# Kernel optimization log

Hardware: AMD Instinct MI355X
Metric: run time of the kernel (lower is better)

The kernel has to match this reference:

```python
import jax, jax.numpy as jnp
import numpy as np

NUM_HEADS = 16
EMBED_DIM = 1024
WINDOW = 8  # attention_window: corner blocks masked with -inf


def _corner_mask(seq_len, w, dtype):
    # zeros everywhere, -inf in top-left [w,w] and bottom-right [w,w] blocks
    m = jnp.zeros((seq_len, seq_len), dtype=dtype)
    neg_inf = jnp.asarray(-jnp.inf, dtype)
    m = m.at[:w, :w].set(neg_inf)
    m = m.at[-w:, -w:].set(neg_inf)
    return m  # [S, S]


def setup_inputs() -> dict:
    key = jax.random.key(0)
    ks = jax.random.split(key, 7)
    B, S, D = 2, 2048, EMBED_DIM
    sc = 0.02
    return {
        "x": jax.random.normal(ks[0], (B, S, D), jnp.float32),
        "Wq": jax.random.normal(ks[1], (D, D), jnp.float32) * sc,
        "bq": jnp.zeros((D,), jnp.float32),
        "Wk": jax.random.normal(ks[2], (D, D), jnp.float32) * sc,
        "bk": jnp.zeros((D,), jnp.float32),
        "Wv": jax.random.normal(ks[3], (D, D), jnp.float32) * sc,
        "bv": jnp.zeros((D,), jnp.float32),
        "global_bias": jnp.zeros((1, NUM_HEADS, 1, 1), jnp.float32),
    }


def reference(x, Wq, bq, Wk, bk, Wv, bv, global_bias):
    B, S, D = x.shape
    H = NUM_HEADS
    hd = D // H
    # linear projections (torch nn.Linear: x @ W.T + b)
    q = (x @ Wq.T + bq).reshape(B, S, H, hd).transpose(0, 2, 1, 3)  # [B,H,S,hd]
    k = (x @ Wk.T + bk).reshape(B, S, H, hd).transpose(0, 2, 1, 3)
    v = (x @ Wv.T + bv).reshape(B, S, H, hd).transpose(0, 2, 1, 3)
    # NOTE: source scales by sqrt(embed_dim), not sqrt(head_dim)
    scores = jnp.einsum("bhqd,bhkd->bhqk", q, k) / jnp.sqrt(jnp.asarray(D, x.dtype))
    scores = scores + global_bias  # learned per-head scalar bias
    scores = scores + _corner_mask(S, WINDOW, x.dtype)  # broadcast [S,S] -> [B,H,S,S]
    attn = jax.nn.softmax(scores, axis=-1)
    ctx = jnp.einsum("bhqk,bhkd->bhqd", attn, v)  # [B,H,S,hd]
    return ctx.transpose(0, 2, 1, 3).reshape(B, S, D)
```

## Files before the change

kernel.cpp:

```cpp
#include <hip/hip_runtime.h>

#define SEQ 2048
#define HDIM 64
#define NH 16
#define EMB 1024

typedef __attribute__((ext_vector_type(8))) short bf16x8;
typedef __attribute__((ext_vector_type(4))) float f32x4;
typedef __attribute__((ext_vector_type(16))) float f32x16;

static __device__ __forceinline__ unsigned short f2bf(float f) {
  unsigned int u = __builtin_bit_cast(unsigned int, f);
  u += 0x7FFF + ((u >> 16) & 1);
  return (unsigned short)(u >> 16);
}

__global__ void cvt_bf16(const float* __restrict__ in, unsigned short* __restrict__ out, int n) {
  int i = (blockIdx.x * blockDim.x + threadIdx.x) * 4;
  if (i + 3 < n) {
    float4 v = *(const float4*)(in + i);
    ushort4 o;
    o.x = f2bf(v.x); o.y = f2bf(v.y); o.z = f2bf(v.z); o.w = f2bf(v.w);
    *(ushort4*)(out + i) = o;
  }
}

__global__ __launch_bounds__(256) void qkv_gemm(
    const unsigned short* __restrict__ xb,
    const unsigned short* __restrict__ wb,
    const float* __restrict__ bq, const float* __restrict__ bk, const float* __restrict__ bv,
    unsigned short* __restrict__ qout, unsigned short* __restrict__ kout,
    unsigned short* __restrict__ vtout)
{
  __shared__ unsigned short As[3][128 * 32];
  __shared__ unsigned short Bs[3][128 * 32];
  const int bid = blockIdx.x;
  const int xg = bid & 7, jj0 = bid >> 3;
  const int cl = jj0 / 24, kk = jj0 % 24;
  const int chunk = xg * 4 + cl;
  const int mg = chunk >> 3, sg = chunk & 7;
  const int mt = mg * 8 + (kk & 7);
  const int strip = sg * 3 + (kk >> 3);
  const int z = strip >> 3;
  const int m0 = mt * 128, n0 = (strip & 7) * 128;

  const unsigned short* Bw = wb + (size_t)z * (EMB * EMB);
  const int tid = threadIdx.x;
  const int w = tid >> 6, l = tid & 63;
  const int wr = w >> 1, wc = w & 1;
  const int lc = l & 15, lg = l >> 4;
  const int NK = EMB / 32;

  f32x4 acc[4][4] = {};

  auto stage = [&](int buf, int kb) {
#pragma unroll
    for (int c = 0; c < 2; ++c) {
      int elem = c * 2048 + w * 512 + l * 8;
      int row = elem >> 5, col = elem & 31;
      __builtin_amdgcn_global_load_lds(
          (const __attribute__((address_space(1))) void*)(xb + (size_t)(m0 + row) * EMB + kb + col),
          (__attribute__((address_space(3))) void*)(&As[buf][c * 2048 + w * 512]), 16, 0, 0);
      __builtin_amdgcn_global_load_lds(
          (const __attribute__((address_space(1))) void*)(Bw + (size_t)(n0 + row) * EMB + kb + col),
          (__attribute__((address_space(3))) void*)(&Bs[buf][c * 2048 + w * 512]), 16, 0, 0);
    }
  };

  stage(0, 0);
  stage(1, 32);

  int cur = 0;
  for (int t = 0; t < NK; ++t) {
    if (t + 1 < NK) {
      asm volatile("s_waitcnt vmcnt(4)" ::: "memory");
    } else {
      asm volatile("s_waitcnt vmcnt(0)" ::: "memory");
    }
    __builtin_amdgcn_s_barrier();
    __builtin_amdgcn_sched_barrier(0);
    bf16x8 am[4], bn[4];
#pragma unroll
    for (int i = 0; i < 4; ++i) {
      am[i] = *(const bf16x8*)(&As[cur][(wr * 64 + i * 16 + lc) * 32 + lg * 8]);
      bn[i] = *(const bf16x8*)(&Bs[cur][(wc * 64 + i * 16 + lc) * 32 + lg * 8]);
    }
    if (t + 2 < NK) {
      int nb = cur + 2; if (nb >= 3) nb -= 3;
      stage(nb, (t + 2) * 32);
    }
#pragma unroll
    for (int i = 0; i < 4; ++i)
#pragma unroll
      for (int j = 0; j < 4; ++j)
        acc[i][j] = __builtin_amdgcn_mfma_f32_16x16x32_bf16(am[i], bn[j], acc[i][j], 0, 0, 0);
    ++cur; if (cur >= 3) cur = 0;
  }

  const float* bias = (z == 0) ? bq : (z == 1) ? bk : bv;
  const float qscale = 0.03125f * 1.44269504f;
  for (int i = 0; i < 4; ++i)
    for (int j = 0; j < 4; ++j)
      for (int r = 0; r < 4; ++r) {
        int m = m0 + wr * 64 + i * 16 + lg * 4 + r;
        int n = n0 + wc * 64 + j * 16 + lc;
        float v = acc[i][j][r] + bias[n];
        if (z == 0) v *= qscale;
        unsigned short o16 = f2bf(v);
        int b = m >> 11, s = m & 2047, h = n >> 6, d = n & 63;
        if (z == 2) {
          int sz = (s & ~12) | ((s & 4) << 1) | ((s & 8) >> 1);
          vtout[(((size_t)b * NH + h) * HDIM + d) * SEQ + sz] = o16;
        } else {
          unsigned short* dst = (z == 0) ? qout : kout;
          dst[(((size_t)b * NH + h) * SEQ + s) * HDIM + d] = o16;
        }
      }
}

__global__ __launch_bounds__(512, 4) void attn(
    const unsigned short* __restrict__ Q,
    const unsigned short* __restrict__ K,
    const unsigned short* __restrict__ VT,
    float* __restrict__ out)
{
  __shared__ __align__(16) unsigned char ldsraw[34816];
  const int g = blockIdx.x;
  const int xcd = g & 7, j0 = g >> 3;
  const int bh = xcd * 4 + (j0 >> 4);
  const int qt = j0 & 15;
  const int b = bh >> 4, h = bh & 15;
  const int tid = threadIdx.x;
  const int half = tid >> 8;
  const int wv4 = (tid >> 6) & 3;
  const int l = tid & 63;
  const int q = l & 31;
  const int hh = l >> 5;
  const int q0 = qt * 128 + wv4 * 32;
  const int NBLK = (SEQ / 2) / 32;

  unsigned short* kv0 = (unsigned short*)ldsraw + half * 8192;
  unsigned short* kv1 = kv0 + 4096;

  const unsigned short* Qp = Q + ((size_t)bh * SEQ + q0) * HDIM;
  const unsigned short* Kp = K + ((size_t)bh * SEQ + (size_t)half * (SEQ / 2)) * HDIM;
  const unsigned short* Vp = VT + (size_t)bh * HDIM * SEQ + (size_t)half * (SEQ / 2);

  bf16x8 qf[4];
#pragma unroll
  for (int c = 0; c < 4; ++c)
    qf[c] = *(const bf16x8*)(Qp + q * HDIM + c * 16 + hh * 8);

  uint4 onesu = make_uint4(0x3F803F80u, 0x3F803F80u, 0x3F803F80u, 0x3F803F80u);
  bf16x8 onesf = __builtin_bit_cast(bf16x8, onesu);

  f32x16 oa = {}, ob = {}, ls = {};
  const bool maskh = (qt == 0) && (wv4 == 0) && (half == 0);
  const bool maskt = (qt == 15) && (wv4 == 3) && (half == 1);

  auto stage = [&](unsigned short* buf, int kbase) {
    __builtin_amdgcn_global_load_lds(
        (const __attribute__((address_space(1))) void*)(Kp + (size_t)(kbase + q) * HDIM + wv4 * 16 + hh * 8),
        (__attribute__((address_space(3))) void*)(buf + wv4 * 512), 16, 0, 0);
    __builtin_amdgcn_global_load_lds(
        (const __attribute__((address_space(1))) void*)(Vp + (size_t)((wv4 >> 1) * 32 + q) * SEQ + kbase + (wv4 & 1) * 16 + hh * 8),
        (__attribute__((address_space(3))) void*)(buf + 2048 + wv4 * 512), 16, 0, 0);
  };

  auto body = [&](const bf16x8* kf, const bf16x8* vf, int t) {
    f32x16 s = {};
#pragma unroll
    for (int c = 0; c < 4; ++c)
      s = __builtin_amdgcn_mfma_f32_32x32x16_bf16(kf[c], qf[c], s, 0, 0, 0);
    if (maskh && t == 0 && q < 8) {
      s[0] = -1e30f; s[1] = -1e30f; s[2] = -1e30f; s[3] = -1e30f;
    }
    if (maskt && t == NBLK - 1 && q >= 24) {
      s[12] = -1e30f; s[13] = -1e30f; s[14] = -1e30f; s[15] = -1e30f;
    }
    float e[16];
#pragma unroll
    for (int jj = 0; jj < 16; ++jj)
      e[jj] = __builtin_amdgcn_exp2f(s[jj]);
    unsigned int P[8];
#pragma unroll
    for (int jj = 0; jj < 8; ++jj)
      asm("v_cvt_pk_bf16_f32 %0, %1, %2" : "=v"(P[jj]) : "v"(e[2 * jj]), "v"(e[2 * jj + 1]));
    uint4 u0q = make_uint4(P[0], P[1], P[2], P[3]);
    uint4 u1q = make_uint4(P[4], P[5], P[6], P[7]);
    bf16x8 pb0 = __builtin_bit_cast(bf16x8, u0q);
    bf16x8 pb1 = __builtin_bit_cast(bf16x8, u1q);
    oa = __builtin_amdgcn_mfma_f32_32x32x16_bf16(vf[0], pb0, oa, 0, 0, 0);
    oa = __builtin_amdgcn_mfma_f32_32x32x16_bf16(vf[1], pb1, oa, 0, 0, 0);
    ob = __builtin_amdgcn_mfma_f32_32x32x16_bf16(vf[2], pb0, ob, 0, 0, 0);
    ob = __builtin_amdgcn_mfma_f32_32x32x16_bf16(vf[3], pb1, ob, 0, 0, 0);
    ls = __builtin_amdgcn_mfma_f32_32x32x16_bf16(onesf, pb0, ls, 0, 0, 0);
    ls = __builtin_amdgcn_mfma_f32_32x32x16_bf16(onesf, pb1, ls, 0, 0, 0);
  };

  stage(kv0, 0);
  asm volatile("s_waitcnt vmcnt(0)" ::: "memory");
  __syncthreads();

  for (int t = 0; t < NBLK; ++t) {
    unsigned short* cur = (t & 1) ? kv1 : kv0;
    if (t + 1 < NBLK) stage((t & 1) ? kv0 : kv1, (t + 1) * 32);
    bf16x8 kf[4], vf[4];
#pragma unroll
    for (int c = 0; c < 4; ++c) kf[c] = *(const bf16x8*)(cur + c * 512 + l * 8);
#pragma unroll
    for (int c = 0; c < 4; ++c) vf[c] = *(const bf16x8*)(cur + 2048 + c * 512 + l * 8);
    body(kf, vf, t);
    asm volatile("s_waitcnt vmcnt(0)" ::: "memory");
    __syncthreads();
  }

  float lrt = ls[0];

  float* smf = (float*)ldsraw;
  if (half == 1) {
    float* p = smf + ((size_t)wv4 * 64 + l) * 33;
#pragma unroll
    for (int j = 0; j < 16; ++j) { p[j] = oa[j]; p[16 + j] = ob[j]; }
    p[32] = lrt;
  }
  __syncthreads();
  if (half == 0) {
    const float* p = smf + ((size_t)wv4 * 64 + l) * 33;
    float inv = __builtin_amdgcn_rcpf(lrt + p[32]);
    float* outp = out + ((size_t)b * SEQ + q0 + q) * EMB + h * HDIM;
#pragma unroll
    for (int qd = 0; qd < 4; ++qd) {
      float4 sa = {(oa[4 * qd] + p[4 * qd]) * inv,
                   (oa[4 * qd + 1] + p[4 * qd + 1]) * inv,
                   (oa[4 * qd + 2] + p[4 * qd + 2]) * inv,
                   (oa[4 * qd + 3] + p[4 * qd + 3]) * inv};
      *(float4*)(outp + 8 * qd + 4 * hh) = sa;
      float4 sb = {(ob[4 * qd] + p[16 + 4 * qd]) * inv,
                   (ob[4 * qd + 1] + p[16 + 4 * qd + 1]) * inv,
                   (ob[4 * qd + 2] + p[16 + 4 * qd + 2]) * inv,
                   (ob[4 * qd + 3] + p[16 + 4 * qd + 3]) * inv};
      *(float4*)(outp + 32 + 8 * qd + 4 * hh) = sb;
    }
  }
}

extern "C" void kernel_launch(void* const* d_in, const int* in_sizes, int n_in,
                              void* d_out, int out_size, void* d_ws, size_t ws_size,
                              hipStream_t stream) {
  const float* x  = (const float*)d_in[0];
  const float* Wq = (const float*)d_in[1];
  const float* bq = (const float*)d_in[2];
  const float* Wk = (const float*)d_in[3];
  const float* bk = (const float*)d_in[4];
  const float* Wv = (const float*)d_in[5];
  const float* bv = (const float*)d_in[6];
  float* out = (float*)d_out;

  char* ws = (char*)d_ws;
  unsigned short* xb   = (unsigned short*)(ws);
  unsigned short* wb   = (unsigned short*)(ws + (8u  << 20));
  unsigned short* qb   = (unsigned short*)(ws + (14u << 20));
  unsigned short* kbuf = (unsigned short*)(ws + (22u << 20));
  unsigned short* vtb  = (unsigned short*)(ws + (30u << 20));

  cvt_bf16<<<4096, 256, 0, stream>>>(x, xb, 2 * SEQ * EMB);
  cvt_bf16<<<1024, 256, 0, stream>>>(Wq, wb, EMB * EMB);
  cvt_bf16<<<1024, 256, 0, stream>>>(Wk, wb + EMB * EMB, EMB * EMB);
  cvt_bf16<<<1024, 256, 0, stream>>>(Wv, wb + 2 * EMB * EMB, EMB * EMB);
  qkv_gemm<<<dim3(768), 256, 0, stream>>>(xb, wb, bq, bk, bv, qb, kbuf, vtb);
  attn<<<dim3(512), 512, 0, stream>>>(qb, kbuf, vtb, out);
}
```

Before: 104.4 us.

## Merge bf16 conversion launches and halve QKV GEMM N-tile to 64

```diff
diff --git a/kernel.cpp b/kernel.cpp
--- a/kernel.cpp
+++ b/kernel.cpp
@@ -15,14 +15,23 @@
   return (unsigned short)(u >> 16);
 }
 
-__global__ void cvt_bf16(const float* __restrict__ in, unsigned short* __restrict__ out, int n) {
+__global__ void cvt_all(const float* __restrict__ x, const float* __restrict__ Wq,
+                        const float* __restrict__ Wk, const float* __restrict__ Wv,
+                        unsigned short* __restrict__ xb, unsigned short* __restrict__ wb) {
+  const int NX = 2 * SEQ * EMB;
+  const int NW = EMB * EMB;
   int i = (blockIdx.x * blockDim.x + threadIdx.x) * 4;
-  if (i + 3 < n) {
-    float4 v = *(const float4*)(in + i);
-    ushort4 o;
-    o.x = f2bf(v.x); o.y = f2bf(v.y); o.z = f2bf(v.z); o.w = f2bf(v.w);
-    *(ushort4*)(out + i) = o;
-  }
+  const float* src;
+  unsigned short* dst;
+  if (i < NX)                { src = x  + i;                 dst = xb + i; }
+  else if (i < NX + NW)      { src = Wq + (i - NX);          dst = wb + (i - NX); }
+  else if (i < NX + 2 * NW)  { src = Wk + (i - NX - NW);     dst = wb + (i - NX); }
+  else if (i < NX + 3 * NW)  { src = Wv + (i - NX - 2 * NW); dst = wb + (i - NX); }
+  else return;
+  float4 v = *(const float4*)src;
+  ushort4 o;
+  o.x = f2bf(v.x); o.y = f2bf(v.y); o.z = f2bf(v.z); o.w = f2bf(v.w);
+  *(ushort4*)dst = o;
 }
 
 __global__ __launch_bounds__(256) void qkv_gemm(
@@ -33,16 +42,16 @@
     unsigned short* __restrict__ vtout)
 {
   __shared__ unsigned short As[3][128 * 32];
-  __shared__ unsigned short Bs[3][128 * 32];
+  __shared__ unsigned short Bs[3][64 * 32];
   const int bid = blockIdx.x;
   const int xg = bid & 7, jj0 = bid >> 3;
-  const int cl = jj0 / 24, kk = jj0 % 24;
+  const int cl = jj0 / 48, kk = jj0 % 48;
   const int chunk = xg * 4 + cl;
   const int mg = chunk >> 3, sg = chunk & 7;
   const int mt = mg * 8 + (kk & 7);
-  const int strip = sg * 3 + (kk >> 3);
-  const int z = strip >> 3;
-  const int m0 = mt * 128, n0 = (strip & 7) * 128;
+  const int strip = sg * 6 + (kk >> 3);
+  const int z = strip >> 4;
+  const int m0 = mt * 128, n0 = (strip & 15) * 64;
 
   const unsigned short* Bw = wb + (size_t)z * (EMB * EMB);
   const int tid = threadIdx.x;
@@ -51,7 +60,7 @@
   const int lc = l & 15, lg = l >> 4;
   const int NK = EMB / 32;
 
-  f32x4 acc[4][4] = {};
+  f32x4 acc[4][2] = {};
 
   auto stage = [&](int buf, int kb) {
 #pragma unroll
@@ -61,9 +70,13 @@
       __builtin_amdgcn_global_load_lds(
           (const __attribute__((address_space(1))) void*)(xb + (size_t)(m0 + row) * EMB + kb + col),
           (__attribute__((address_space(3))) void*)(&As[buf][c * 2048 + w * 512]), 16, 0, 0);
+    }
+    {
+      int elem = w * 512 + l * 8;
+      int row = elem >> 5, col = elem & 31;
       __builtin_amdgcn_global_load_lds(
           (const __attribute__((address_space(1))) void*)(Bw + (size_t)(n0 + row) * EMB + kb + col),
-          (__attribute__((address_space(3))) void*)(&Bs[buf][c * 2048 + w * 512]), 16, 0, 0);
+          (__attribute__((address_space(3))) void*)(&Bs[buf][w * 512]), 16, 0, 0);
     }
   };
 
@@ -73,18 +86,19 @@
   int cur = 0;
   for (int t = 0; t < NK; ++t) {
     if (t + 1 < NK) {
-      asm volatile("s_waitcnt vmcnt(4)" ::: "memory");
+      asm volatile("s_waitcnt vmcnt(3)" ::: "memory");
     } else {
       asm volatile("s_waitcnt vmcnt(0)" ::: "memory");
     }
     __builtin_amdgcn_s_barrier();
     __builtin_amdgcn_sched_barrier(0);
-    bf16x8 am[4], bn[4];
-#pragma unroll
-    for (int i = 0; i < 4; ++i) {
+    bf16x8 am[4], bn[2];
+#pragma unroll
+    for (int i = 0; i < 4; ++i)
       am[i] = *(const bf16x8*)(&As[cur][(wr * 64 + i * 16 + lc) * 32 + lg * 8]);
-      bn[i] = *(const bf16x8*)(&Bs[cur][(wc * 64 + i * 16 + lc) * 32 + lg * 8]);
-    }
+#pragma unroll
+    for (int j = 0; j < 2; ++j)
+      bn[j] = *(const bf16x8*)(&Bs[cur][(wc * 32 + j * 16 + lc) * 32 + lg * 8]);
     if (t + 2 < NK) {
       int nb = cur + 2; if (nb >= 3) nb -= 3;
       stage(nb, (t + 2) * 32);
@@ -92,7 +106,7 @@
 #pragma unroll
     for (int i = 0; i < 4; ++i)
 #pragma unroll
-      for (int j = 0; j < 4; ++j)
+      for (int j = 0; j < 2; ++j)
         acc[i][j] = __builtin_amdgcn_mfma_f32_16x16x32_bf16(am[i], bn[j], acc[i][j], 0, 0, 0);
     ++cur; if (cur >= 3) cur = 0;
   }
@@ -100,10 +114,10 @@
   const float* bias = (z == 0) ? bq : (z == 1) ? bk : bv;
   const float qscale = 0.03125f * 1.44269504f;
   for (int i = 0; i < 4; ++i)
-    for (int j = 0; j < 4; ++j)
+    for (int j = 0; j < 2; ++j)
       for (int r = 0; r < 4; ++r) {
         int m = m0 + wr * 64 + i * 16 + lg * 4 + r;
-        int n = n0 + wc * 64 + j * 16 + lc;
+        int n = n0 + wc * 32 + j * 16 + lc;
         float v = acc[i][j][r] + bias[n];
         if (z == 0) v *= qscale;
         unsigned short o16 = f2bf(v);
@@ -264,10 +278,7 @@
   unsigned short* kbuf = (unsigned short*)(ws + (22u << 20));
   unsigned short* vtb  = (unsigned short*)(ws + (30u << 20));
 
-  cvt_bf16<<<4096, 256, 0, stream>>>(x, xb, 2 * SEQ * EMB);
-  cvt_bf16<<<1024, 256, 0, stream>>>(Wq, wb, EMB * EMB);
-  cvt_bf16<<<1024, 256, 0, stream>>>(Wk, wb + EMB * EMB, EMB * EMB);
-  cvt_bf16<<<1024, 256, 0, stream>>>(Wv, wb + 2 * EMB * EMB, EMB * EMB);
-  qkv_gemm<<<dim3(768), 256, 0, stream>>>(xb, wb, bq, bk, bv, qb, kbuf, vtb);
+  cvt_all<<<7168, 256, 0, stream>>>(x, Wq, Wk, Wv, xb, wb);
+  qkv_gemm<<<dim3(1536), 256, 0, stream>>>(xb, wb, bq, bk, bv, qb, kbuf, vtb);
   attn<<<dim3(512), 512, 0, stream>>>(qb, kbuf, vtb, out);
 }
```

Measured after the change: 105.3 us. No clear change (+0.8%).
